# Performance work log

Measured on AMD Instinct MI355X. Metric: run time of the kernel, lower is better.

Reference implementation:

```python
import jax, jax.numpy as jnp
import numpy as np

B, S, D = 1, 2048, 1024          # batch, seq, hidden_size
E, K, F = 8, 2, 1408             # n_routed_experts, top_k, moe_intermediate_size
NS = 2                           # n_shared_experts
SCALE = 2.5                      # routed_scaling_factor (norm_topk_prob=True)


def setup_inputs() -> dict:
    key = jax.random.key(0)
    ks = jax.random.split(key, 8)
    s = 0.02
    return {
        "hidden_states": jax.random.normal(ks[0], (B, S, D), jnp.float32),
        "gate_w": jax.random.normal(ks[1], (E, D), jnp.float32) * s,
        "w_gate": jax.random.normal(ks[2], (E, D, F), jnp.float32) * s,
        "w_up": jax.random.normal(ks[3], (E, D, F), jnp.float32) * s,
        "w_down": jax.random.normal(ks[4], (E, F, D), jnp.float32) * s,
        "sw_gate": jax.random.normal(ks[5], (D, F * NS), jnp.float32) * s,
        "sw_up": jax.random.normal(ks[6], (D, F * NS), jnp.float32) * s,
        "sw_down": jax.random.normal(ks[7], (F * NS, D), jnp.float32) * s,
    }


def _swiglu_mlp(x, wg, wu, wd):
    # down( silu(gate(x)) * up(x) )
    return (jax.nn.silu(x @ wg) * (x @ wu)) @ wd


def reference(hidden_states, gate_w, w_gate, w_up, w_down, sw_gate, sw_up, sw_down):
    identity = hidden_states
    x = hidden_states.reshape(-1, hidden_states.shape[-1])  # [T, D]
    T = x.shape[0]

    # --- MoEGate (softmax scoring, greedy top-k, normalized + scaled) ---
    logits = x.astype(jnp.float32) @ gate_w.astype(jnp.float32).T  # [T, E]
    scores = jax.nn.softmax(logits, axis=-1)
    topk_w, topk_i = jax.lax.top_k(scores, K)                      # [T, K]
    topk_w = topk_w / (topk_w.sum(-1, keepdims=True) + 1e-20) * SCALE

    # Dense combine weights [T, E]: topk weight where routed, 0 elsewhere.
    combine = jnp.zeros((T, E), jnp.float32).at[
        jnp.arange(T)[:, None], topk_i
    ].set(topk_w)

    # --- Routed experts as grouped GEMMs (same math as sort/dispatch loop) ---
    g = jax.nn.silu(jnp.einsum('td,edf->etf', x, w_gate)) \
        * jnp.einsum('td,edf->etf', x, w_up)                       # [E, T, F]
    expert_out = jnp.einsum('etf,efd->etd', g, w_down)             # [E, T, D]
    y = jnp.einsum('te,etd->td', combine, expert_out).astype(x.dtype)
    y = y.reshape(identity.shape)

    # --- Shared expert ---
    return y + _swiglu_mlp(identity, sw_gate, sw_up, sw_down)
```

## Files before the change

kernel.cpp:

```cpp
#include <hip/hip_runtime.h>
#include <hip/hip_bf16.h>
#include <stdint.h>

#define TT 2048
#define DD 1024
#define NE 8
#define FR 1408
#define FS 2816
#define RSCALE 2.5f
#define NSLOT (TT * 2)

typedef __attribute__((ext_vector_type(8))) short bf16x8;
typedef __attribute__((ext_vector_type(4))) float f32x4;

__device__ __forceinline__ short f2bf(float f) {
  uint32_t u = __builtin_bit_cast(uint32_t, f);
  u = (u + 0x7fffu + ((u >> 16) & 1u)) >> 16;
  return (short)(uint16_t)u;
}

__global__ void cast_kernel(const float* __restrict__ in, short* __restrict__ out, int n) {
  int i = (blockIdx.x * blockDim.x + threadIdx.x) * 4;
  if (i >= n) return;
  float4 v = *(const float4*)(in + i);
  short4 o;
  o.x = f2bf(v.x); o.y = f2bf(v.y); o.z = f2bf(v.z); o.w = f2bf(v.w);
  *(short4*)(out + i) = o;
}

__global__ void __launch_bounds__(256) tcast_kernel(const float* __restrict__ in,
                                                    short* __restrict__ out,
                                                    int K, int N, int64_t zin, int64_t zout) {
  const int z = blockIdx.z;
  in += (int64_t)z * zin;
  out += (int64_t)z * zout;
  __shared__ float tile[32][33];
  const int k0 = blockIdx.y * 32, n0 = blockIdx.x * 32;
  const int tx = threadIdx.x, ty = threadIdx.y;
#pragma unroll
  for (int i = 0; i < 4; ++i)
    tile[ty * 4 + i][tx] = in[(int64_t)(k0 + ty * 4 + i) * N + n0 + tx];
  __syncthreads();
#pragma unroll
  for (int i = 0; i < 4; ++i)
    out[(int64_t)(n0 + ty * 4 + i) * K + k0 + tx] = f2bf(tile[tx][ty * 4 + i]);
}

__global__ void gate_kernel(const float* __restrict__ x, const float* __restrict__ gw,
                            int* __restrict__ te, float* __restrict__ tw) {
  int t = blockIdx.x;
  int lane = threadIdx.x;
  const float* xr = x + (size_t)t * DD + lane * 16;
  float4 xv[4];
#pragma unroll
  for (int i = 0; i < 4; ++i) xv[i] = *(const float4*)(xr + i * 4);
  float p[NE];
#pragma unroll
  for (int e = 0; e < NE; ++e) {
    const float* gr = gw + (size_t)e * DD + lane * 16;
    float s = 0.f;
#pragma unroll
    for (int i = 0; i < 4; ++i) {
      float4 g = *(const float4*)(gr + i * 4);
      s += xv[i].x * g.x + xv[i].y * g.y + xv[i].z * g.z + xv[i].w * g.w;
    }
    p[e] = s;
  }
#pragma unroll
  for (int off = 32; off >= 1; off >>= 1) {
#pragma unroll
    for (int e = 0; e < NE; ++e) p[e] += __shfl_xor(p[e], off);
  }
  float mx = p[0];
#pragma unroll
  for (int e = 1; e < NE; ++e) mx = fmaxf(mx, p[e]);
  float s = 0.f, sc[NE];
#pragma unroll
  for (int e = 0; e < NE; ++e) { sc[e] = expf(p[e] - mx); s += sc[e]; }
  float inv = 1.f / s;
#pragma unroll
  for (int e = 0; e < NE; ++e) sc[e] *= inv;
  int e1 = 0;
#pragma unroll
  for (int e = 1; e < NE; ++e) if (sc[e] > sc[e1]) e1 = e;
  int e2 = (e1 == 0) ? 1 : 0;
#pragma unroll
  for (int e = 0; e < NE; ++e) if (e != e1 && sc[e] > sc[e2]) e2 = e;
  float w1 = sc[e1], w2 = sc[e2];
  float k = RSCALE / (w1 + w2 + 1e-20f);
  if (lane == 0) {
    te[t * 2] = e1;     tw[t * 2] = w1 * k;
    te[t * 2 + 1] = e2; tw[t * 2 + 1] = w2 * k;
  }
}

__global__ void __launch_bounds__(1024) scatter_kernel(const int* __restrict__ te,
                                                       const float* __restrict__ tw,
                                                       int* __restrict__ cnt, int* __restrict__ off,
                                                       int* __restrict__ eidx, float* __restrict__ wslot) {
  __shared__ int lcnt[NE], loff[NE], lrun[NE];
  const int tid = threadIdx.x;
  if (tid < NE) lcnt[tid] = 0;
  __syncthreads();
  for (int s = tid; s < NSLOT; s += 1024) atomicAdd(&lcnt[te[s]], 1);
  __syncthreads();
  if (tid == 0) {
    int acc = 0;
    for (int e = 0; e < NE; ++e) { loff[e] = acc; lrun[e] = acc; acc += lcnt[e]; }
  }
  __syncthreads();
  for (int s = tid; s < NSLOT; s += 1024) {
    int e = te[s];
    int p = atomicAdd(&lrun[e], 1);
    eidx[p] = s >> 1;
    wslot[p] = tw[s];
  }
  if (tid < NE) { cnt[tid] = lcnt[tid]; off[tid] = loff[tid]; }
}

__device__ __forceinline__ void stage32(const short* __restrict__ g, int64_t ld,
                                        short* l, int wave, int lane) {
#pragma unroll
  for (int i = 0; i < 2; ++i) {
    int c = i * 256 + wave * 64 + lane;
    __builtin_amdgcn_global_load_lds(
        (const __attribute__((address_space(1))) void*)(g + (int64_t)(c >> 2) * ld + (c & 3) * 8),
        (__attribute__((address_space(3))) void*)(l + (i * 256 + wave * 64) * 8),
        16, 0, 0);
  }
}

template <int MODE>
__global__ void __launch_bounds__(256) moe_gemm(
    const short* __restrict__ Ab, int lda,
    const short* __restrict__ B0b, const short* __restrict__ B1b, int ldb,
    int K,
    short* __restrict__ Hb, int ldh,
    float* __restrict__ Ob) {
  const int brow = blockIdx.y * 128;
  const int bcol = blockIdx.x * 128;

  __shared__ __align__(16) short lA[128 * 32];
  __shared__ __align__(16) short lB0[128 * 32];
  __shared__ __align__(16) short lB1[(MODE == 0) ? 128 * 32 : 8];

  const int tid = threadIdx.x;
  const int lane = tid & 63;
  const int wave = tid >> 6;
  const int wr = wave >> 1, wc = wave & 1;

  f32x4 acc0[4][4];
  f32x4 acc1[(MODE == 0) ? 4 : 1][(MODE == 0) ? 4 : 1];
#pragma unroll
  for (int m = 0; m < 4; ++m)
#pragma unroll
    for (int n = 0; n < 4; ++n) {
      acc0[m][n] = (f32x4){0.f, 0.f, 0.f, 0.f};
      if constexpr (MODE == 0) acc1[m][n] = (f32x4){0.f, 0.f, 0.f, 0.f};
    }

  const short* Abase = Ab + (int64_t)brow * lda;
  const short* B0base = B0b + (int64_t)bcol * ldb;
  const short* B1base = (MODE == 0) ? (B1b + (int64_t)bcol * ldb) : nullptr;

  for (int k0 = 0; k0 < K; k0 += 32) {
    stage32(Abase + k0, lda, lA, wave, lane);
    stage32(B0base + k0, ldb, lB0, wave, lane);
    if constexpr (MODE == 0) stage32(B1base + k0, ldb, lB1, wave, lane);
    __syncthreads();
#pragma unroll
    for (int m = 0; m < 4; ++m) {
      bf16x8 af = *(const bf16x8*)&lA[(wr * 64 + m * 16 + (lane & 15)) * 32 + (lane >> 4) * 8];
#pragma unroll
      for (int n = 0; n < 4; ++n) {
        bf16x8 b0 = *(const bf16x8*)&lB0[(wc * 64 + n * 16 + (lane & 15)) * 32 + (lane >> 4) * 8];
        acc0[m][n] = __builtin_amdgcn_mfma_f32_16x16x32_bf16(af, b0, acc0[m][n], 0, 0, 0);
        if constexpr (MODE == 0) {
          bf16x8 b1 = *(const bf16x8*)&lB1[(wc * 64 + n * 16 + (lane & 15)) * 32 + (lane >> 4) * 8];
          acc1[m][n] = __builtin_amdgcn_mfma_f32_16x16x32_bf16(af, b1, acc1[m][n], 0, 0, 0);
        }
      }
    }
    __syncthreads();
  }

#pragma unroll
  for (int m = 0; m < 4; ++m)
#pragma unroll
    for (int n = 0; n < 4; ++n)
#pragma unroll
      for (int r = 0; r < 4; ++r) {
        int row = brow + wr * 64 + m * 16 + (lane >> 4) * 4 + r;
        int col = bcol + wc * 64 + n * 16 + (lane & 15);
        float g = acc0[m][n][r];
        if constexpr (MODE == 0) {
          float u = acc1[m][n][r];
          Hb[(int64_t)row * ldh + col] = f2bf(g / (1.f + __expf(-g)) * u);
        } else {
          Ob[(int64_t)row * DD + col] = g;
        }
      }
}

__global__ void __launch_bounds__(256) gu_sparse(
    const short* __restrict__ Xb,
    const short* __restrict__ wgT, const short* __restrict__ wuT,
    short* __restrict__ Hr,
    const int* __restrict__ cnt, const int* __restrict__ off,
    const int* __restrict__ eidx) {
  const int z = blockIdx.z;
  const int c = cnt[z];
  const int m0 = blockIdx.y * 128;
  if (m0 >= c) return;
  const int base = off[z];
  const int bcol = blockIdx.x * 128;

  __shared__ __align__(16) short lA[128 * 32];
  __shared__ __align__(16) short lB0[128 * 32];
  __shared__ __align__(16) short lB1[128 * 32];

  const int tid = threadIdx.x;
  const int lane = tid & 63;
  const int wave = tid >> 6;
  const int wr = wave >> 1, wc = wave & 1;

  const short* aptr[2];
#pragma unroll
  for (int i = 0; i < 2; ++i) {
    int cl = i * 256 + wave * 64 + lane;
    int r = cl >> 2;
    int sv = m0 + r; if (sv >= c) sv = c - 1;
    aptr[i] = Xb + (int64_t)eidx[base + sv] * DD + (cl & 3) * 8;
  }

  f32x4 acc0[4][4], acc1[4][4];
#pragma unroll
  for (int m = 0; m < 4; ++m)
#pragma unroll
    for (int n = 0; n < 4; ++n) {
      acc0[m][n] = (f32x4){0.f, 0.f, 0.f, 0.f};
      acc1[m][n] = (f32x4){0.f, 0.f, 0.f, 0.f};
    }

  const short* B0base = wgT + (int64_t)z * FR * DD + (int64_t)bcol * DD;
  const short* B1base = wuT + (int64_t)z * FR * DD + (int64_t)bcol * DD;

  for (int k0 = 0; k0 < DD; k0 += 32) {
#pragma unroll
    for (int i = 0; i < 2; ++i)
      __builtin_amdgcn_global_load_lds(
          (const __attribute__((address_space(1))) void*)(aptr[i] + k0),
          (__attribute__((address_space(3))) void*)(lA + (i * 256 + wave * 64) * 8),
          16, 0, 0);
    stage32(B0base + k0, DD, lB0, wave, lane);
    stage32(B1base + k0, DD, lB1, wave, lane);
    __syncthreads();
#pragma unroll
    for (int m = 0; m < 4; ++m) {
      bf16x8 af = *(const bf16x8*)&lA[(wr * 64 + m * 16 + (lane & 15)) * 32 + (lane >> 4) * 8];
#pragma unroll
      for (int n = 0; n < 4; ++n) {
        bf16x8 b0 = *(const bf16x8*)&lB0[(wc * 64 + n * 16 + (lane & 15)) * 32 + (lane >> 4) * 8];
        acc0[m][n] = __builtin_amdgcn_mfma_f32_16x16x32_bf16(af, b0, acc0[m][n], 0, 0, 0);
        bf16x8 b1 = *(const bf16x8*)&lB1[(wc * 64 + n * 16 + (lane & 15)) * 32 + (lane >> 4) * 8];
        acc1[m][n] = __builtin_amdgcn_mfma_f32_16x16x32_bf16(af, b1, acc1[m][n], 0, 0, 0);
      }
    }
    __syncthreads();
  }

#pragma unroll
  for (int m = 0; m < 4; ++m)
#pragma unroll
    for (int n = 0; n < 4; ++n)
#pragma unroll
      for (int r = 0; r < 4; ++r) {
        int rl = wr * 64 + m * 16 + (lane >> 4) * 4 + r;
        int sv = m0 + rl;
        if (sv < c) {
          int col = bcol + wc * 64 + n * 16 + (lane & 15);
          float g = acc0[m][n][r], u = acc1[m][n][r];
          Hr[(int64_t)(base + sv) * FR + col] = f2bf(g / (1.f + __expf(-g)) * u);
        }
      }
}

__global__ void __launch_bounds__(256) down_sparse(
    const short* __restrict__ Hr,
    const short* __restrict__ wdT,
    float* __restrict__ out,
    const int* __restrict__ cnt, const int* __restrict__ off,
    const int* __restrict__ eidx, const float* __restrict__ wslot) {
  const int z = blockIdx.z;
  const int c = cnt[z];
  const int m0 = blockIdx.y * 128;
  if (m0 >= c) return;
  const int base = off[z];
  const int bcol = blockIdx.x * 128;

  __shared__ __align__(16) short lA[128 * 32];
  __shared__ __align__(16) short lB0[128 * 32];
  __shared__ int lTok[128];
  __shared__ float lW[128];

  const int tid = threadIdx.x;
  const int lane = tid & 63;
  const int wave = tid >> 6;
  const int wr = wave >> 1, wc = wave & 1;

  if (tid < 128) {
    int sv = m0 + tid;
    if (sv < c) { lTok[tid] = eidx[base + sv]; lW[tid] = wslot[base + sv]; }
    else lW[tid] = 0.f;
  }

  f32x4 acc0[4][4];
#pragma unroll
  for (int m = 0; m < 4; ++m)
#pragma unroll
    for (int n = 0; n < 4; ++n) acc0[m][n] = (f32x4){0.f, 0.f, 0.f, 0.f};

  const int64_t arow0 = base + m0;
  const short* B0base = wdT + (int64_t)z * DD * FR + (int64_t)bcol * FR;

  for (int k0 = 0; k0 < FR; k0 += 32) {
#pragma unroll
    for (int i = 0; i < 2; ++i) {
      int cl = i * 256 + wave * 64 + lane;
      int r = cl >> 2;
      int sv = m0 + r; if (sv >= c) sv = c - 1;
      __builtin_amdgcn_global_load_lds(
          (const __attribute__((address_space(1))) void*)(Hr + (int64_t)(base + sv) * FR + k0 + (cl & 3) * 8),
          (__attribute__((address_space(3))) void*)(lA + (i * 256 + wave * 64) * 8),
          16, 0, 0);
    }
    stage32(B0base + k0, FR, lB0, wave, lane);
    __syncthreads();
#pragma unroll
    for (int m = 0; m < 4; ++m) {
      bf16x8 af = *(const bf16x8*)&lA[(wr * 64 + m * 16 + (lane & 15)) * 32 + (lane >> 4) * 8];
#pragma unroll
      for (int n = 0; n < 4; ++n) {
        bf16x8 b0 = *(const bf16x8*)&lB0[(wc * 64 + n * 16 + (lane & 15)) * 32 + (lane >> 4) * 8];
        acc0[m][n] = __builtin_amdgcn_mfma_f32_16x16x32_bf16(af, b0, acc0[m][n], 0, 0, 0);
      }
    }
    __syncthreads();
  }

#pragma unroll
  for (int m = 0; m < 4; ++m)
#pragma unroll
    for (int n = 0; n < 4; ++n)
#pragma unroll
      for (int r = 0; r < 4; ++r) {
        int rl = wr * 64 + m * 16 + (lane >> 4) * 4 + r;
        if (m0 + rl < c) {
          int col = bcol + wc * 64 + n * 16 + (lane & 15);
          atomicAdd(&out[(int64_t)lTok[rl] * DD + col], lW[rl] * acc0[m][n][r]);
        }
      }
}

extern "C" void kernel_launch(void* const* d_in, const int* in_sizes, int n_in,
                              void* d_out, int out_size, void* d_ws, size_t ws_size,
                              hipStream_t stream) {
  const float* x       = (const float*)d_in[0];
  const float* gw      = (const float*)d_in[1];
  const float* w_gate  = (const float*)d_in[2];
  const float* w_up    = (const float*)d_in[3];
  const float* w_down  = (const float*)d_in[4];
  const float* sw_gate = (const float*)d_in[5];
  const float* sw_up   = (const float*)d_in[6];
  const float* sw_down = (const float*)d_in[7];
  float* out = (float*)d_out;

  char* ws = (char*)d_ws;
  int*   te    = (int*)ws;    ws += NSLOT * 4;
  float* tw    = (float*)ws;  ws += NSLOT * 4;
  int*   cnt   = (int*)ws;    ws += 64 * 4;
  int*   off   = (int*)ws;    ws += 64 * 4;
  int*   eidx  = (int*)ws;    ws += NSLOT * 4;
  float* wslot = (float*)ws;  ws += NSLOT * 4;
  ws = (char*)(((uintptr_t)ws + 255) & ~(uintptr_t)255);
  short* Xb   = (short*)ws;  ws += (size_t)TT * DD * 2;
  short* Hs   = (short*)ws;  ws += (size_t)TT * FS * 2;
  short* Hr   = (short*)ws;  ws += (size_t)NSLOT * FR * 2;
  short* wgT  = (short*)ws;  ws += (size_t)NE * FR * DD * 2;
  short* wuT  = (short*)ws;  ws += (size_t)NE * FR * DD * 2;
  short* wdT  = (short*)ws;  ws += (size_t)NE * DD * FR * 2;
  short* swgT = (short*)ws;  ws += (size_t)FS * DD * 2;
  short* swuT = (short*)ws;  ws += (size_t)FS * DD * 2;
  short* swdT = (short*)ws;

  cast_kernel<<<dim3((TT * DD) / 1024), dim3(256), 0, stream>>>(x, Xb, TT * DD);
  gate_kernel<<<dim3(TT), dim3(64), 0, stream>>>(x, gw, te, tw);
  scatter_kernel<<<dim3(1), dim3(1024), 0, stream>>>(te, tw, cnt, off, eidx, wslot);
  dim3 tb(32, 8);
  tcast_kernel<<<dim3(FR / 32, DD / 32, NE), tb, 0, stream>>>(w_gate, wgT, DD, FR, (int64_t)DD * FR, (int64_t)FR * DD);
  tcast_kernel<<<dim3(FR / 32, DD / 32, NE), tb, 0, stream>>>(w_up,   wuT, DD, FR, (int64_t)DD * FR, (int64_t)FR * DD);
  tcast_kernel<<<dim3(DD / 32, FR / 32, NE), tb, 0, stream>>>(w_down, wdT, FR, DD, (int64_t)FR * DD, (int64_t)DD * FR);
  tcast_kernel<<<dim3(FS / 32, DD / 32, 1),  tb, 0, stream>>>(sw_gate, swgT, DD, FS, 0, 0);
  tcast_kernel<<<dim3(FS / 32, DD / 32, 1),  tb, 0, stream>>>(sw_up,   swuT, DD, FS, 0, 0);
  tcast_kernel<<<dim3(DD / 32, FS / 32, 1),  tb, 0, stream>>>(sw_down, swdT, FS, DD, 0, 0);
  moe_gemm<0><<<dim3(FS / 128, TT / 128), dim3(256), 0, stream>>>(
      Xb, DD, swgT, swuT, DD, DD, Hs, FS, nullptr);
  gu_sparse<<<dim3(FR / 128, TT / 128, NE), dim3(256), 0, stream>>>(
      Xb, wgT, wuT, Hr, cnt, off, eidx);
  moe_gemm<1><<<dim3(DD / 128, TT / 128), dim3(256), 0, stream>>>(
      Hs, FS, swdT, nullptr, FS, FS, nullptr, 0, out);
  down_sparse<<<dim3(DD / 128, TT / 128, NE), dim3(256), 0, stream>>>(
      Hr, wdT, out, cnt, off, eidx, wslot);
}
```

Before: 499.9 us.

## Double-buffer LDS tiles in GEMMs and merge weight transpose-cast launches

Every GEMM kernel (dense shared-expert GEMMs and the sparse gate/up and down kernels) now keeps two LDS buffers and issues the async global-to-LDS load for the next K-slice before computing on the current one, with one barrier per iteration instead of two. This is meant to hide global load latency behind MFMA work. The weight transpose-cast kernel is also changed: gate/up pairs are merged into single launches and the output is written as 4-element vector stores. The cost is doubled LDS per block, which may reduce occupancy, especially for the three-buffer gate/up kernels.

```diff
diff --git a/kernel.cpp b/kernel.cpp
--- a/kernel.cpp
+++ b/kernel.cpp
@@ -9,6 +9,7 @@
 #define FS 2816
 #define RSCALE 2.5f
 #define NSLOT (TT * 2)
+#define TSH 4096
 
 typedef __attribute__((ext_vector_type(8))) short bf16x8;
 typedef __attribute__((ext_vector_type(4))) float f32x4;
@@ -28,22 +29,28 @@
   *(short4*)(out + i) = o;
 }
 
-__global__ void __launch_bounds__(256) tcast_kernel(const float* __restrict__ in,
-                                                    short* __restrict__ out,
-                                                    int K, int N, int64_t zin, int64_t zout) {
-  const int z = blockIdx.z;
-  in += (int64_t)z * zin;
-  out += (int64_t)z * zout;
+__global__ void __launch_bounds__(256) tcastV(const float* __restrict__ in0,
+                                              const float* __restrict__ in1,
+                                              short* __restrict__ out0, short* __restrict__ out1,
+                                              int K, int N, int64_t zin, int64_t zout, int nz) {
+  int z = blockIdx.z;
+  const float* in;
+  short* out;
+  if (z < nz) { in = in0 + (int64_t)z * zin; out = out0 + (int64_t)z * zout; }
+  else        { int zz = z - nz; in = in1 + (int64_t)zz * zin; out = out1 + (int64_t)zz * zout; }
   __shared__ float tile[32][33];
   const int k0 = blockIdx.y * 32, n0 = blockIdx.x * 32;
-  const int tx = threadIdx.x, ty = threadIdx.y;
+  const int tid = threadIdx.x;
+  const int lr = tid >> 5, lc = tid & 31;
 #pragma unroll
   for (int i = 0; i < 4; ++i)
-    tile[ty * 4 + i][tx] = in[(int64_t)(k0 + ty * 4 + i) * N + n0 + tx];
-  __syncthreads();
-#pragma unroll
-  for (int i = 0; i < 4; ++i)
-    out[(int64_t)(n0 + ty * 4 + i) * K + k0 + tx] = f2bf(tile[tx][ty * 4 + i]);
+    tile[lr + i * 8][lc] = in[(int64_t)(k0 + lr + i * 8) * N + n0 + lc];
+  __syncthreads();
+  const int nl = tid >> 3, kq = (tid & 7) * 4;
+  short4 o;
+  o.x = f2bf(tile[kq + 0][nl]); o.y = f2bf(tile[kq + 1][nl]);
+  o.z = f2bf(tile[kq + 2][nl]); o.w = f2bf(tile[kq + 3][nl]);
+  *(short4*)&out[(int64_t)(n0 + nl) * K + k0 + kq] = o;
 }
 
 __global__ void gate_kernel(const float* __restrict__ x, const float* __restrict__ gw,
@@ -140,9 +147,9 @@
   const int brow = blockIdx.y * 128;
   const int bcol = blockIdx.x * 128;
 
-  __shared__ __align__(16) short lA[128 * 32];
-  __shared__ __align__(16) short lB0[128 * 32];
-  __shared__ __align__(16) short lB1[(MODE == 0) ? 128 * 32 : 8];
+  __shared__ __align__(16) short lA[2 * TSH];
+  __shared__ __align__(16) short lB0[2 * TSH];
+  __shared__ __align__(16) short lB1[(MODE == 0) ? 2 * TSH : 8];
 
   const int tid = threadIdx.x;
   const int lane = tid & 63;
@@ -163,25 +170,35 @@
   const short* B0base = B0b + (int64_t)bcol * ldb;
   const short* B1base = (MODE == 0) ? (B1b + (int64_t)bcol * ldb) : nullptr;
 
+  auto STAGE = [&](int buf, int k0) {
+    stage32(Abase + k0, lda, lA + buf * TSH, wave, lane);
+    stage32(B0base + k0, ldb, lB0 + buf * TSH, wave, lane);
+    if constexpr (MODE == 0) stage32(B1base + k0, ldb, lB1 + buf * TSH, wave, lane);
+  };
+
+  STAGE(0, 0);
+  __syncthreads();
+  int cur = 0;
   for (int k0 = 0; k0 < K; k0 += 32) {
-    stage32(Abase + k0, lda, lA, wave, lane);
-    stage32(B0base + k0, ldb, lB0, wave, lane);
-    if constexpr (MODE == 0) stage32(B1base + k0, ldb, lB1, wave, lane);
-    __syncthreads();
+    if (k0 + 32 < K) STAGE(cur ^ 1, k0 + 32);
+    const short* A_ = lA + cur * TSH;
+    const short* B0_ = lB0 + cur * TSH;
+    const short* B1_ = lB1 + cur * TSH;
 #pragma unroll
     for (int m = 0; m < 4; ++m) {
-      bf16x8 af = *(const bf16x8*)&lA[(wr * 64 + m * 16 + (lane & 15)) * 32 + (lane >> 4) * 8];
+      bf16x8 af = *(const bf16x8*)&A_[(wr * 64 + m * 16 + (lane & 15)) * 32 + (lane >> 4) * 8];
 #pragma unroll
       for (int n = 0; n < 4; ++n) {
-        bf16x8 b0 = *(const bf16x8*)&lB0[(wc * 64 + n * 16 + (lane & 15)) * 32 + (lane >> 4) * 8];
+        bf16x8 b0 = *(const bf16x8*)&B0_[(wc * 64 + n * 16 + (lane & 15)) * 32 + (lane >> 4) * 8];
         acc0[m][n] = __builtin_amdgcn_mfma_f32_16x16x32_bf16(af, b0, acc0[m][n], 0, 0, 0);
         if constexpr (MODE == 0) {
-          bf16x8 b1 = *(const bf16x8*)&lB1[(wc * 64 + n * 16 + (lane & 15)) * 32 + (lane >> 4) * 8];
+          bf16x8 b1 = *(const bf16x8*)&B1_[(wc * 64 + n * 16 + (lane & 15)) * 32 + (lane >> 4) * 8];
           acc1[m][n] = __builtin_amdgcn_mfma_f32_16x16x32_bf16(af, b1, acc1[m][n], 0, 0, 0);
         }
       }
     }
     __syncthreads();
+    cur ^= 1;
   }
 
 #pragma unroll
@@ -215,9 +232,9 @@
   const int base = off[z];
   const int bcol = blockIdx.x * 128;
 
-  __shared__ __align__(16) short lA[128 * 32];
-  __shared__ __align__(16) short lB0[128 * 32];
-  __shared__ __align__(16) short lB1[128 * 32];
+  __shared__ __align__(16) short lA[2 * TSH];
+  __shared__ __align__(16) short lB0[2 * TSH];
+  __shared__ __align__(16) short lB1[2 * TSH];
 
   const int tid = threadIdx.x;
   const int lane = tid & 63;
@@ -245,28 +262,38 @@
   const short* B0base = wgT + (int64_t)z * FR * DD + (int64_t)bcol * DD;
   const short* B1base = wuT + (int64_t)z * FR * DD + (int64_t)bcol * DD;
 
-  for (int k0 = 0; k0 < DD; k0 += 32) {
+  auto STAGE = [&](int buf, int k0) {
 #pragma unroll
     for (int i = 0; i < 2; ++i)
       __builtin_amdgcn_global_load_lds(
           (const __attribute__((address_space(1))) void*)(aptr[i] + k0),
-          (__attribute__((address_space(3))) void*)(lA + (i * 256 + wave * 64) * 8),
+          (__attribute__((address_space(3))) void*)(lA + buf * TSH + (i * 256 + wave * 64) * 8),
           16, 0, 0);
-    stage32(B0base + k0, DD, lB0, wave, lane);
-    stage32(B1base + k0, DD, lB1, wave, lane);
+    stage32(B0base + k0, DD, lB0 + buf * TSH, wave, lane);
+    stage32(B1base + k0, DD, lB1 + buf * TSH, wave, lane);
+  };
+
+  STAGE(0, 0);
+  __syncthreads();
+  int cur = 0;
+  for (int k0 = 0; k0 < DD; k0 += 32) {
+    if (k0 + 32 < DD) STAGE(cur ^ 1, k0 + 32);
+    const short* A_ = lA + cur * TSH;
+    const short* B0_ = lB0 + cur * TSH;
+    const short* B1_ = lB1 + cur * TSH;
+#pragma unroll
+    for (int m = 0; m < 4; ++m) {
+      bf16x8 af = *(const bf16x8*)&A_[(wr * 64 + m * 16 + (lane & 15)) * 32 + (lane >> 4) * 8];
+#pragma unroll
+      for (int n = 0; n < 4; ++n) {
+        bf16x8 b0 = *(const bf16x8*)&B0_[(wc * 64 + n * 16 + (lane & 15)) * 32 + (lane >> 4) * 8];
+        acc0[m][n] = __builtin_amdgcn_mfma_f32_16x16x32_bf16(af, b0, acc0[m][n], 0, 0, 0);
+        bf16x8 b1 = *(const bf16x8*)&B1_[(wc * 64 + n * 16 + (lane & 15)) * 32 + (lane >> 4) * 8];
+        acc1[m][n] = __builtin_amdgcn_mfma_f32_16x16x32_bf16(af, b1, acc1[m][n], 0, 0, 0);
+      }
+    }
     __syncthreads();
-#pragma unroll
-    for (int m = 0; m < 4; ++m) {
-      bf16x8 af = *(const bf16x8*)&lA[(wr * 64 + m * 16 + (lane & 15)) * 32 + (lane >> 4) * 8];
-#pragma unroll
-      for (int n = 0; n < 4; ++n) {
-        bf16x8 b0 = *(const bf16x8*)&lB0[(wc * 64 + n * 16 + (lane & 15)) * 32 + (lane >> 4) * 8];
-        acc0[m][n] = __builtin_amdgcn_mfma_f32_16x16x32_bf16(af, b0, acc0[m][n], 0, 0, 0);
-        bf16x8 b1 = *(const bf16x8*)&lB1[(wc * 64 + n * 16 + (lane & 15)) * 32 + (lane >> 4) * 8];
-        acc1[m][n] = __builtin_amdgcn_mfma_f32_16x16x32_bf16(af, b1, acc1[m][n], 0, 0, 0);
-      }
-    }
-    __syncthreads();
+    cur ^= 1;
   }
 
 #pragma unroll
@@ -298,8 +325,8 @@
   const int base = off[z];
   const int bcol = blockIdx.x * 128;
 
-  __shared__ __align__(16) short lA[128 * 32];
-  __shared__ __align__(16) short lB0[128 * 32];
+  __shared__ __align__(16) short lA[2 * TSH];
+  __shared__ __align__(16) short lB0[2 * TSH];
   __shared__ int lTok[128];
   __shared__ float lW[128];
 
@@ -320,10 +347,9 @@
 #pragma unroll
     for (int n = 0; n < 4; ++n) acc0[m][n] = (f32x4){0.f, 0.f, 0.f, 0.f};
 
-  const int64_t arow0 = base + m0;
   const short* B0base = wdT + (int64_t)z * DD * FR + (int64_t)bcol * FR;
 
-  for (int k0 = 0; k0 < FR; k0 += 32) {
+  auto STAGE = [&](int buf, int k0) {
 #pragma unroll
     for (int i = 0; i < 2; ++i) {
       int cl = i * 256 + wave * 64 + lane;
@@ -331,21 +357,30 @@
       int sv = m0 + r; if (sv >= c) sv = c - 1;
       __builtin_amdgcn_global_load_lds(
           (const __attribute__((address_space(1))) void*)(Hr + (int64_t)(base + sv) * FR + k0 + (cl & 3) * 8),
-          (__attribute__((address_space(3))) void*)(lA + (i * 256 + wave * 64) * 8),
+          (__attribute__((address_space(3))) void*)(lA + buf * TSH + (i * 256 + wave * 64) * 8),
           16, 0, 0);
     }
-    stage32(B0base + k0, FR, lB0, wave, lane);
+    stage32(B0base + k0, FR, lB0 + buf * TSH, wave, lane);
+  };
+
+  STAGE(0, 0);
+  __syncthreads();
+  int cur = 0;
+  for (int k0 = 0; k0 < FR; k0 += 32) {
+    if (k0 + 32 < FR) STAGE(cur ^ 1, k0 + 32);
+    const short* A_ = lA + cur * TSH;
+    const short* B0_ = lB0 + cur * TSH;
+#pragma unroll
+    for (int m = 0; m < 4; ++m) {
+      bf16x8 af = *(const bf16x8*)&A_[(wr * 64 + m * 16 + (lane & 15)) * 32 + (lane >> 4) * 8];
+#pragma unroll
+      for (int n = 0; n < 4; ++n) {
+        bf16x8 b0 = *(const bf16x8*)&B0_[(wc * 64 + n * 16 + (lane & 15)) * 32 + (lane >> 4) * 8];
+        acc0[m][n] = __builtin_amdgcn_mfma_f32_16x16x32_bf16(af, b0, acc0[m][n], 0, 0, 0);
+      }
+    }
     __syncthreads();
-#pragma unroll
-    for (int m = 0; m < 4; ++m) {
-      bf16x8 af = *(const bf16x8*)&lA[(wr * 64 + m * 16 + (lane & 15)) * 32 + (lane >> 4) * 8];
-#pragma unroll
-      for (int n = 0; n < 4; ++n) {
-        bf16x8 b0 = *(const bf16x8*)&lB0[(wc * 64 + n * 16 + (lane & 15)) * 32 + (lane >> 4) * 8];
-        acc0[m][n] = __builtin_amdgcn_mfma_f32_16x16x32_bf16(af, b0, acc0[m][n], 0, 0, 0);
-      }
-    }
-    __syncthreads();
+    cur ^= 1;
   }
 
 #pragma unroll
@@ -396,13 +431,14 @@
   cast_kernel<<<dim3((TT * DD) / 1024), dim3(256), 0, stream>>>(x, Xb, TT * DD);
   gate_kernel<<<dim3(TT), dim3(64), 0, stream>>>(x, gw, te, tw);
   scatter_kernel<<<dim3(1), dim3(1024), 0, stream>>>(te, tw, cnt, off, eidx, wslot);
-  dim3 tb(32, 8);
-  tcast_kernel<<<dim3(FR / 32, DD / 32, NE), tb, 0, stream>>>(w_gate, wgT, DD, FR, (int64_t)DD * FR, (int64_t)FR * DD);
-  tcast_kernel<<<dim3(FR / 32, DD / 32, NE), tb, 0, stream>>>(w_up,   wuT, DD, FR, (int64_t)DD * FR, (int64_t)FR * DD);
-  tcast_kernel<<<dim3(DD / 32, FR / 32, NE), tb, 0, stream>>>(w_down, wdT, FR, DD, (int64_t)FR * DD, (int64_t)DD * FR);
-  tcast_kernel<<<dim3(FS / 32, DD / 32, 1),  tb, 0, stream>>>(sw_gate, swgT, DD, FS, 0, 0);
-  tcast_kernel<<<dim3(FS / 32, DD / 32, 1),  tb, 0, stream>>>(sw_up,   swuT, DD, FS, 0, 0);
-  tcast_kernel<<<dim3(DD / 32, FS / 32, 1),  tb, 0, stream>>>(sw_down, swdT, FS, DD, 0, 0);
+  tcastV<<<dim3(FR / 32, DD / 32, 2 * NE), dim3(256), 0, stream>>>(
+      w_gate, w_up, wgT, wuT, DD, FR, (int64_t)DD * FR, (int64_t)FR * DD, NE);
+  tcastV<<<dim3(DD / 32, FR / 32, NE), dim3(256), 0, stream>>>(
+      w_down, w_down, wdT, wdT, FR, DD, (int64_t)FR * DD, (int64_t)DD * FR, NE);
+  tcastV<<<dim3(FS / 32, DD / 32, 2), dim3(256), 0, stream>>>(
+      sw_gate, sw_up, swgT, swuT, DD, FS, 0, 0, 1);
+  tcastV<<<dim3(DD / 32, FS / 32, 1), dim3(256), 0, stream>>>(
+      sw_down, sw_down, swdT, swdT, FS, DD, 0, 0, 1);
   moe_gemm<0><<<dim3(FS / 128, TT / 128), dim3(256), 0, stream>>>(
       Xb, DD, swgT, swuT, DD, DD, Hs, FS, nullptr);
   gu_sparse<<<dim3(FR / 128, TT / 128, NE), dim3(256), 0, stream>>>(
```

Result: faster. 480.4 us (-3.9%).
